# Kernel tuning notes

Hardware: AMD Instinct MI355X
Metric: run time of the kernel (lower is better)

The kernel has to match this reference:

```python
import math
import jax, jax.numpy as jnp
import numpy as np

B, L, D_MODEL = 2, 2048, 1024
N_HEAD, HEAD_DIM = 16, 64
ATT_SCALE = 1.0  # divisor is sqrt(head_dim ** attention_scale)


def setup_inputs() -> dict:
    key = jax.random.key(0)
    ks = jax.random.split(key, 6)
    HD = N_HEAD * HEAD_DIM
    # Xavier-uniform style init for projection weights (stored as [in, out])
    def xavier(k, fan_in, fan_out):
        lim = math.sqrt(6.0 / (fan_in + fan_out))
        return jax.random.uniform(k, (fan_in, fan_out), jnp.float32, -lim, lim)
    return {
        "x":  jax.random.normal(ks[0], (B, L, D_MODEL), jnp.float32),
        "Wq": xavier(ks[1], D_MODEL, HD), "bq": jnp.zeros((HD,), jnp.float32),
        "Wk": xavier(ks[2], D_MODEL, HD), "bk": jnp.zeros((HD,), jnp.float32),
        "Wv": xavier(ks[3], D_MODEL, HD), "bv": jnp.zeros((HD,), jnp.float32),
        "Wo": xavier(ks[4], HD, D_MODEL),
        "bo": jax.random.uniform(ks[5], (D_MODEL,), jnp.float32, -1.0 / math.sqrt(HD), 1.0 / math.sqrt(HD)),
    }


def reference(x, Wq, bq, Wk, bk, Wv, bv, Wo, bo):
    b, l, _ = x.shape
    # QKV projections -> [B, L, H, Dh]
    q = (x @ Wq + bq).reshape(b, l, N_HEAD, HEAD_DIM)
    k = (x @ Wk + bk).reshape(b, l, N_HEAD, HEAD_DIM)
    v = (x @ Wv + bv).reshape(b, l, N_HEAD, HEAD_DIM)
    scale = 1.0 / math.sqrt(HEAD_DIM ** ATT_SCALE)
    # Unnormalized (no softmax) attention: (Q K^T / sqrt(Dh)) V
    scores = jnp.einsum("blhd,bmhd->bhlm", q, k) * scale  # [B,H,L,L]
    attn = jnp.einsum("bhlm,bmhd->blhd", scores, v)        # [B,L,H,Dh]
    out = attn.reshape(b, l, N_HEAD * HEAD_DIM) @ Wo + bo  # dispatcher
    return out
```

## Files before the change

### kernel.cpp

```cpp
#include <hip/hip_runtime.h>
#include <stdint.h>

#define B_ 2
#define L_ 2048
#define DM 1024
#define NH 16
#define DH 64
#define M_ (B_*L_)
#define NQKV 3072

typedef short short8 __attribute__((ext_vector_type(8)));
typedef float f32x4 __attribute__((ext_vector_type(4)));

__device__ __forceinline__ unsigned short f2b(float f) {
    union { float f; unsigned int u; } v; v.f = f;
    unsigned int u = v.u;
    return (unsigned short)((u + 0x7fffu + ((u >> 16) & 1u)) >> 16);
}

__device__ __forceinline__ void gld_lds16(const void* g, void* l) {
    __builtin_amdgcn_global_load_lds(
        (const __attribute__((address_space(1))) void*)g,
        (__attribute__((address_space(3))) void*)l, 16, 0, 0);
}

__global__ __launch_bounds__(256)
void setup_kernel(const float* __restrict__ x,
                  const float* __restrict__ Wq, const float* __restrict__ Wk,
                  const float* __restrict__ Wv, const float* __restrict__ Wo,
                  const float* __restrict__ bq, const float* __restrict__ bk,
                  const float* __restrict__ bv,
                  unsigned short* __restrict__ xb, unsigned short* __restrict__ WqkvT,
                  unsigned short* __restrict__ WoT, float* __restrict__ biasq,
                  float* __restrict__ KtV)
{
    __shared__ float tile[32][33];
    const int bid = blockIdx.x;
    const int t = threadIdx.x;

    if (bid < 2048) {
        int i = (bid * 256 + t) * 8;
        float4 a0 = *(const float4*)(x + i);
        float4 a1 = *(const float4*)(x + i + 4);
        uint4 p;
        p.x = (unsigned)f2b(a0.x) | ((unsigned)f2b(a0.y) << 16);
        p.y = (unsigned)f2b(a0.z) | ((unsigned)f2b(a0.w) << 16);
        p.z = (unsigned)f2b(a1.x) | ((unsigned)f2b(a1.y) << 16);
        p.w = (unsigned)f2b(a1.z) | ((unsigned)f2b(a1.w) << 16);
        *(uint4*)(xb + i) = p;
    } else if (bid < 2048 + 4096) {
        int wb = bid - 2048;
        int wi = wb >> 10;
        int tid = wb & 1023;
        const float* W = (wi == 0) ? Wq : (wi == 1) ? Wk : (wi == 2) ? Wv : Wo;
        float s = (wi == 1) ? 0.125f : 1.0f;
        int n0 = (tid & 31) * 32, k0 = (tid >> 5) * 32;
        int r = t >> 3, c4 = (t & 7) << 2;
        float4 v = *(const float4*)(W + (size_t)(k0 + r) * DM + n0 + c4);
        tile[r][c4+0] = v.x; tile[r][c4+1] = v.y; tile[r][c4+2] = v.z; tile[r][c4+3] = v.w;
        __syncthreads();
        uint2 o;
        o.x = (unsigned)f2b(tile[c4+0][r]*s) | ((unsigned)f2b(tile[c4+1][r]*s) << 16);
        o.y = (unsigned)f2b(tile[c4+2][r]*s) | ((unsigned)f2b(tile[c4+3][r]*s) << 16);
        int f = n0 + r;
        size_t drow;
        unsigned short* dst;
        if (wi == 0)      { dst = WqkvT; drow = f; }
        else if (wi == 1) { dst = WqkvT; drow = 1024 + (f >> 6) * 128 + (f & 63); }
        else if (wi == 2) { dst = WqkvT; drow = 1024 + (f >> 6) * 128 + 64 + (f & 63); }
        else              { dst = WoT;   drow = f; }
        *(uint2*)(dst + drow * DM + k0 + c4) = o;
    } else if (bid < 2048 + 4096 + 12) {
        int n = (bid - 6144) * 256 + t;
        float v;
        if (n < 1024) v = bq[n];
        else {
            int kv = (n - 1024) >> 7, r = (n - 1024) & 127;
            v = (r < 64) ? 0.125f * bk[kv * 64 + r] : bv[kv * 64 + (r - 64)];
        }
        biasq[n] = v;
    } else {
        int i = ((bid - 6156) * 256 + t) * 4;
        float4 z; z.x = z.y = z.z = z.w = 0.f;
        *(float4*)(KtV + i) = z;
    }
}

__global__ __launch_bounds__(256)
void qkv_fused_kernel(const unsigned short* __restrict__ A,
                      const unsigned short* __restrict__ Bt,
                      const float* __restrict__ biasq,
                      unsigned short* __restrict__ Qb,
                      float* __restrict__ KtV)
{
    __shared__ __align__(16) char smem[34816];
    unsigned short* As = (unsigned short*)smem;
    unsigned short* Bs = (unsigned short*)(smem + 8192);

    const int bid = blockIdx.x;
    const int xcd = bid & 7, local = bid >> 3;
    const int mt = xcd * 4 + (local & 3);
    const int nt = local >> 2;
    const int m0 = mt * 128, n0 = nt * 128;

    const int t = threadIdx.x;
    const int w = t >> 6, lane = t & 63;
    const int quad = lane >> 4, l16 = lane & 15;
    const int wm = w >> 1, wn = w & 1;

    f32x4 acc[4][4];
    #pragma unroll
    for (int i = 0; i < 4; i++)
        #pragma unroll
        for (int j = 0; j < 4; j++)
            #pragma unroll
            for (int r = 0; r < 4; r++) acc[i][j][r] = 0.f;

    const int srow = t >> 2;
    const int schunk = t & 3;

    for (int kk = 0; kk < DM; kk += 32) {
        #pragma unroll
        for (int p = 0; p < 2; p++) {
            int row = p * 64 + srow;
            int g = schunk ^ ((row >> 1) & 3);
            gld_lds16(A  + (size_t)(m0 + row) * DM + kk + g * 8,
                      (char*)As + p * 4096 + w * 1024);
            gld_lds16(Bt + (size_t)(n0 + row) * DM + kk + g * 8,
                      (char*)Bs + p * 4096 + w * 1024);
        }
        __syncthreads();

        short8 afr[4], bfr[4];
        #pragma unroll
        for (int i = 0; i < 4; i++) {
            int am = wm * 64 + i * 16 + l16;
            afr[i] = *(const short8*)((const char*)As + am * 64 + ((quad ^ ((am >> 1) & 3)) << 4));
            int bn = wn * 64 + i * 16 + l16;
            bfr[i] = *(const short8*)((const char*)Bs + bn * 64 + ((quad ^ ((bn >> 1) & 3)) << 4));
        }
        #pragma unroll
        for (int i = 0; i < 4; i++)
            #pragma unroll
            for (int j = 0; j < 4; j++)
                acc[i][j] = __builtin_amdgcn_mfma_f32_16x16x32_bf16(afr[i], bfr[j], acc[i][j], 0, 0, 0);
        __syncthreads();
    }

    #pragma unroll
    for (int j = 0; j < 4; j++) {
        float bv = biasq[n0 + wn * 64 + j * 16 + l16];
        #pragma unroll
        for (int i = 0; i < 4; i++)
            #pragma unroll
            for (int r = 0; r < 4; r++) acc[i][j][r] += bv;
    }

    if (nt < 8) {
        #pragma unroll
        for (int j = 0; j < 4; j++) {
            int col = n0 + wn * 64 + j * 16 + l16;
            #pragma unroll
            for (int i = 0; i < 4; i++) {
                #pragma unroll
                for (int r = 0; r < 4; r++) {
                    int row = m0 + wm * 64 + i * 16 + quad * 4 + r;
                    Qb[(size_t)row * DM + col] = f2b(acc[i][j][r]);
                }
            }
        }
        return;
    }

    const int h  = nt - 8;
    const int bh = (m0 >> 11) * NH + h;
    unsigned short (*Xt)[136] = (unsigned short (*)[136])smem;

    #pragma unroll
    for (int j = 0; j < 4; j++) {
        int c = wn * 64 + j * 16 + l16;
        #pragma unroll
        for (int i = 0; i < 4; i++) {
            int l0 = wm * 64 + i * 16 + quad * 4;
            uint2 o;
            o.x = (unsigned)f2b(acc[i][j][0]) | ((unsigned)f2b(acc[i][j][1]) << 16);
            o.y = (unsigned)f2b(acc[i][j][2]) | ((unsigned)f2b(acc[i][j][3]) << 16);
            *(uint2*)&Xt[c][l0] = o;
        }
    }
    __syncthreads();

    f32x4 kacc[4];
    #pragma unroll
    for (int j = 0; j < 4; j++)
        #pragma unroll
        for (int r = 0; r < 4; r++) kacc[j][r] = 0.f;

    #pragma unroll
    for (int ks = 0; ks < 4; ks++) {
        short8 af = *(const short8*)&Xt[w * 16 + l16][ks * 32 + quad * 8];
        #pragma unroll
        for (int j = 0; j < 4; j++) {
            short8 bfr = *(const short8*)&Xt[64 + j * 16 + l16][ks * 32 + quad * 8];
            kacc[j] = __builtin_amdgcn_mfma_f32_16x16x32_bf16(af, bfr, kacc[j], 0, 0, 0);
        }
    }

    float* dst = KtV + (size_t)bh * 64 * 64;
    #pragma unroll
    for (int j = 0; j < 4; j++) {
        int col = j * 16 + l16;
        #pragma unroll
        for (int r = 0; r < 4; r++) {
            int row = w * 16 + quad * 4 + r;
            atomicAdd(dst + row * 64 + col, kacc[j][r]);
        }
    }
}

__global__ __launch_bounds__(256)
void zmat_kernel(const unsigned short* __restrict__ WoT, const float* __restrict__ KtV,
                 unsigned short* __restrict__ ZT)
{
    __shared__ __align__(16) unsigned short Asl[64][72];
    __shared__ __align__(16) unsigned short Bsl[64][72];

    const int bh = blockIdx.x, nt0 = blockIdx.y;
    const int b = bh >> 4, h = bh & 15;
    const int t = threadIdx.x;
    const int wave = t >> 6, lane = t & 63;
    const int quad = lane >> 4, l16 = lane & 15;
    const int n0 = nt0 * 64;
    const int row = t >> 2, c0 = (t & 3) << 4;

    const unsigned short* ap = WoT + (size_t)(n0 + row) * DM + h * DH + c0;
    *(uint4*)&Asl[row][c0]     = *(const uint4*)ap;
    *(uint4*)&Asl[row][c0 + 8] = *(const uint4*)(ap + 8);

    const float* kp = KtV + ((size_t)bh * 64 + row) * 64 + c0;
    #pragma unroll
    for (int j = 0; j < 16; j++) Bsl[row][c0 + j] = f2b(kp[j]);
    __syncthreads();

    f32x4 acc[4];
    #pragma unroll
    for (int i = 0; i < 4; i++)
        #pragma unroll
        for (int r = 0; r < 4; r++) acc[i][r] = 0.f;

    #pragma unroll
    for (int ks = 0; ks < 2; ks++) {
        short8 af = *(const short8*)&Asl[wave * 16 + l16][ks * 32 + quad * 8];
        #pragma unroll
        for (int nt = 0; nt < 4; nt++) {
            short8 bfr = *(const short8*)&Bsl[nt * 16 + l16][ks * 32 + quad * 8];
            acc[nt] = __builtin_amdgcn_mfma_f32_16x16x32_bf16(af, bfr, acc[nt], 0, 0, 0);
        }
    }

    unsigned short* zb = ZT + (size_t)b * 1024 * 1024 + (size_t)h * DH;
    #pragma unroll
    for (int nt = 0; nt < 4; nt++) {
        int col = nt * 16 + l16;
        #pragma unroll
        for (int r = 0; r < 4; r++) {
            int zr = n0 + wave * 16 + quad * 4 + r;
            zb[(size_t)zr * 1024 + col] = f2b(acc[nt][r]);
        }
    }
}

__global__ __launch_bounds__(256)
void out_gemm_kernel(const unsigned short* __restrict__ A,
                     const unsigned short* __restrict__ Bt,
                     const float* __restrict__ bias,
                     float* __restrict__ C)
{
    constexpr int BN = 64, MI = 2, MJ = 4;
    __shared__ __align__(16) unsigned short As[128 * 32];
    __shared__ __align__(16) unsigned short Bs[BN * 32];

    const int bid = blockIdx.x;
    const int xcd = bid & 7, local = bid >> 3;
    const int mt = xcd * 4 + (local & 3);
    const int nt = local >> 2;
    const int m0 = mt * 128, n0 = nt * 64;

    const int t = threadIdx.x;
    const int w = t >> 6, lane = t & 63;
    const int quad = lane >> 4, l16 = lane & 15;

    const unsigned short* Btb = Bt + (size_t)(m0 >> 11) * 1024 * 1024;

    f32x4 acc[MI][MJ];
    #pragma unroll
    for (int i = 0; i < MI; i++)
        #pragma unroll
        for (int j = 0; j < MJ; j++)
            #pragma unroll
            for (int r = 0; r < 4; r++) acc[i][j][r] = 0.f;

    const int srow = t >> 2;
    const int schunk = t & 3;

    for (int kk = 0; kk < DM; kk += 32) {
        #pragma unroll
        for (int p = 0; p < 2; p++) {
            int row = p * 64 + srow;
            int g = schunk ^ ((row >> 1) & 3);
            gld_lds16(A + (size_t)(m0 + row) * DM + kk + g * 8,
                      (char*)As + p * 4096 + w * 1024);
        }
        {
            int row = srow;
            int g = schunk ^ ((row >> 1) & 3);
            gld_lds16(Btb + (size_t)(n0 + row) * DM + kk + g * 8,
                      (char*)Bs + w * 1024);
        }
        __syncthreads();

        short8 afr[MI], bfr[MJ];
        #pragma unroll
        for (int i = 0; i < MI; i++) {
            int am = w * 32 + i * 16 + l16;
            afr[i] = *(const short8*)((const char*)As + am * 64 + ((quad ^ ((am >> 1) & 3)) << 4));
        }
        #pragma unroll
        for (int j = 0; j < MJ; j++) {
            int bn = j * 16 + l16;
            bfr[j] = *(const short8*)((const char*)Bs + bn * 64 + ((quad ^ ((bn >> 1) & 3)) << 4));
        }
        #pragma unroll
        for (int i = 0; i < MI; i++)
            #pragma unroll
            for (int j = 0; j < MJ; j++)
                acc[i][j] = __builtin_amdgcn_mfma_f32_16x16x32_bf16(afr[i], bfr[j], acc[i][j], 0, 0, 0);
        __syncthreads();
    }

    #pragma unroll
    for (int j = 0; j < MJ; j++) {
        int col = n0 + j * 16 + l16;
        float bv = bias[col];
        #pragma unroll
        for (int i = 0; i < MI; i++) {
            #pragma unroll
            for (int r = 0; r < 4; r++) {
                int row = m0 + w * 32 + i * 16 + quad * 4 + r;
                C[(size_t)row * DM + col] = acc[i][j][r] + bv;
            }
        }
    }
}


extern "C" void kernel_launch(void* const* d_in, const int* in_sizes, int n_in,
                              void* d_out, int out_size, void* d_ws, size_t ws_size,
                              hipStream_t stream)
{
    const float* x  = (const float*)d_in[0];
    const float* Wq = (const float*)d_in[1];
    const float* bq = (const float*)d_in[2];
    const float* Wk = (const float*)d_in[3];
    const float* bk = (const float*)d_in[4];
    const float* Wv = (const float*)d_in[5];
    const float* bv = (const float*)d_in[6];
    const float* Wo = (const float*)d_in[7];
    const float* bo = (const float*)d_in[8];

    char* ws = (char*)d_ws;
    unsigned short* xb    = (unsigned short*)(ws);
    unsigned short* WqkvT = (unsigned short*)(ws + (size_t)8  * 1024 * 1024);
    unsigned short* WoT   = (unsigned short*)(ws + (size_t)14 * 1024 * 1024);
    float*          biasq = (float*)         (ws + (size_t)16 * 1024 * 1024);
    unsigned short* Qb    = (unsigned short*)(ws + (size_t)17 * 1024 * 1024);
    unsigned short* ZT    = (unsigned short*)(ws + (size_t)25 * 1024 * 1024);
    float*          KtV   = (float*)         (ws + (size_t)29 * 1024 * 1024);

    setup_kernel<<<6284, 256, 0, stream>>>(x, Wq, Wk, Wv, Wo, bq, bk, bv,
                                           xb, WqkvT, WoT, biasq, KtV);

    qkv_fused_kernel<<<768, 256, 0, stream>>>(xb, WqkvT, biasq, Qb, KtV);

    zmat_kernel<<<dim3(B_ * NH, 16), 256, 0, stream>>>(WoT, KtV, ZT);

    out_gemm_kernel<<<512, 256, 0, stream>>>(Qb, ZT, bo, (float*)d_out);
}
```

Before: 147.0 us.

## Use 128x128 split-K tiles in output GEMM with atomic accumulation onto bias-initialized output

The output GEMM now uses 128x128 tiles with a 2-way split over K, so each block computes a 4x4 MFMA grid per wave with more operand reuse while the block count stays at 512. Partial sums are accumulated into the output with float atomics, and the setup kernel pre-fills the output with the broadcast bias. This trades fewer redundant operand loads per FLOP for atomic traffic on 4M outputs, an extra full-output write in setup, and non-deterministic summation order.

```diff
diff --git a/kernel.cpp b/kernel.cpp
--- a/kernel.cpp
+++ b/kernel.cpp
@@ -29,10 +29,10 @@
                   const float* __restrict__ Wq, const float* __restrict__ Wk,
                   const float* __restrict__ Wv, const float* __restrict__ Wo,
                   const float* __restrict__ bq, const float* __restrict__ bk,
-                  const float* __restrict__ bv,
+                  const float* __restrict__ bv, const float* __restrict__ bo,
                   unsigned short* __restrict__ xb, unsigned short* __restrict__ WqkvT,
                   unsigned short* __restrict__ WoT, float* __restrict__ biasq,
-                  float* __restrict__ KtV)
+                  float* __restrict__ KtV, float* __restrict__ outp)
 {
     __shared__ float tile[32][33];
     const int bid = blockIdx.x;
@@ -79,10 +79,13 @@
             v = (r < 64) ? 0.125f * bk[kv * 64 + r] : bv[kv * 64 + (r - 64)];
         }
         biasq[n] = v;
-    } else {
+    } else if (bid < 2048 + 4096 + 12 + 128) {
         int i = ((bid - 6156) * 256 + t) * 4;
         float4 z; z.x = z.y = z.z = z.w = 0.f;
         *(float4*)(KtV + i) = z;
+    } else {
+        int i = ((bid - 6284) * 256 + t) * 4;
+        *(float4*)(outp + i) = *(const float4*)(bo + (i & 1023));
     }
 }
 
@@ -273,81 +276,74 @@
 __global__ __launch_bounds__(256)
 void out_gemm_kernel(const unsigned short* __restrict__ A,
                      const unsigned short* __restrict__ Bt,
-                     const float* __restrict__ bias,
                      float* __restrict__ C)
 {
-    constexpr int BN = 64, MI = 2, MJ = 4;
     __shared__ __align__(16) unsigned short As[128 * 32];
-    __shared__ __align__(16) unsigned short Bs[BN * 32];
+    __shared__ __align__(16) unsigned short Bs[128 * 32];
 
     const int bid = blockIdx.x;
     const int xcd = bid & 7, local = bid >> 3;
-    const int mt = xcd * 4 + (local & 3);
-    const int nt = local >> 2;
-    const int m0 = mt * 128, n0 = nt * 64;
+    const int kh = local & 1;
+    const int mt = xcd * 4 + ((local >> 1) & 3);
+    const int nt = local >> 3;
+    const int m0 = mt * 128, n0 = nt * 128;
+    const int kbase = kh * 512;
 
     const int t = threadIdx.x;
     const int w = t >> 6, lane = t & 63;
     const int quad = lane >> 4, l16 = lane & 15;
-
-    const unsigned short* Btb = Bt + (size_t)(m0 >> 11) * 1024 * 1024;
-
-    f32x4 acc[MI][MJ];
-    #pragma unroll
-    for (int i = 0; i < MI; i++)
-        #pragma unroll
-        for (int j = 0; j < MJ; j++)
+    const int wm = w >> 1, wn = w & 1;
+
+    const unsigned short* Btb = Bt + (size_t)(mt >> 4) * 1024 * 1024;
+
+    f32x4 acc[4][4];
+    #pragma unroll
+    for (int i = 0; i < 4; i++)
+        #pragma unroll
+        for (int j = 0; j < 4; j++)
             #pragma unroll
             for (int r = 0; r < 4; r++) acc[i][j][r] = 0.f;
 
     const int srow = t >> 2;
     const int schunk = t & 3;
 
-    for (int kk = 0; kk < DM; kk += 32) {
+    for (int kk = kbase; kk < kbase + 512; kk += 32) {
         #pragma unroll
         for (int p = 0; p < 2; p++) {
             int row = p * 64 + srow;
             int g = schunk ^ ((row >> 1) & 3);
-            gld_lds16(A + (size_t)(m0 + row) * DM + kk + g * 8,
+            gld_lds16(A   + (size_t)(m0 + row) * DM + kk + g * 8,
                       (char*)As + p * 4096 + w * 1024);
-        }
-        {
-            int row = srow;
-            int g = schunk ^ ((row >> 1) & 3);
             gld_lds16(Btb + (size_t)(n0 + row) * DM + kk + g * 8,
-                      (char*)Bs + w * 1024);
-        }
-        __syncthreads();
-
-        short8 afr[MI], bfr[MJ];
-        #pragma unroll
-        for (int i = 0; i < MI; i++) {
-            int am = w * 32 + i * 16 + l16;
+                      (char*)Bs + p * 4096 + w * 1024);
+        }
+        __syncthreads();
+
+        short8 afr[4], bfr[4];
+        #pragma unroll
+        for (int i = 0; i < 4; i++) {
+            int am = wm * 64 + i * 16 + l16;
             afr[i] = *(const short8*)((const char*)As + am * 64 + ((quad ^ ((am >> 1) & 3)) << 4));
-        }
-        #pragma unroll
-        for (int j = 0; j < MJ; j++) {
-            int bn = j * 16 + l16;
-            bfr[j] = *(const short8*)((const char*)Bs + bn * 64 + ((quad ^ ((bn >> 1) & 3)) << 4));
-        }
-        #pragma unroll
-        for (int i = 0; i < MI; i++)
-            #pragma unroll
-            for (int j = 0; j < MJ; j++)
+            int bn = wn * 64 + i * 16 + l16;
+            bfr[i] = *(const short8*)((const char*)Bs + bn * 64 + ((quad ^ ((bn >> 1) & 3)) << 4));
+        }
+        #pragma unroll
+        for (int i = 0; i < 4; i++)
+            #pragma unroll
+            for (int j = 0; j < 4; j++)
                 acc[i][j] = __builtin_amdgcn_mfma_f32_16x16x32_bf16(afr[i], bfr[j], acc[i][j], 0, 0, 0);
         __syncthreads();
     }
 
     #pragma unroll
-    for (int j = 0; j < MJ; j++) {
-        int col = n0 + j * 16 + l16;
-        float bv = bias[col];
-        #pragma unroll
-        for (int i = 0; i < MI; i++) {
+    for (int j = 0; j < 4; j++) {
+        int col = n0 + wn * 64 + j * 16 + l16;
+        #pragma unroll
+        for (int i = 0; i < 4; i++) {
             #pragma unroll
             for (int r = 0; r < 4; r++) {
-                int row = m0 + w * 32 + i * 16 + quad * 4 + r;
-                C[(size_t)row * DM + col] = acc[i][j][r] + bv;
+                int row = m0 + wm * 64 + i * 16 + quad * 4 + r;
+                atomicAdd(C + (size_t)row * DM + col, acc[i][j][r]);
             }
         }
     }
@@ -377,12 +373,12 @@
     unsigned short* ZT    = (unsigned short*)(ws + (size_t)25 * 1024 * 1024);
     float*          KtV   = (float*)         (ws + (size_t)29 * 1024 * 1024);
 
-    setup_kernel<<<6284, 256, 0, stream>>>(x, Wq, Wk, Wv, Wo, bq, bk, bv,
-                                           xb, WqkvT, WoT, biasq, KtV);
+    setup_kernel<<<7308, 256, 0, stream>>>(x, Wq, Wk, Wv, Wo, bq, bk, bv, bo,
+                                           xb, WqkvT, WoT, biasq, KtV, (float*)d_out);
 
     qkv_fused_kernel<<<768, 256, 0, stream>>>(xb, WqkvT, biasq, Qb, KtV);
 
     zmat_kernel<<<dim3(B_ * NH, 16), 256, 0, stream>>>(WoT, KtV, ZT);
 
-    out_gemm_kernel<<<512, 256, 0, stream>>>(Qb, ZT, bo, (float*)d_out);
-}
+    out_gemm_kernel<<<512, 256, 0, stream>>>(Qb, ZT, (float*)d_out);
+}
```

Result: slower. 164.8 us (+12.1%).

## Fuse four kernels into one persistent kernel with grid barriers

Applied to the files above, without the earlier changes.

Replaces the setup, QKV GEMM, Z-matrix and output GEMM launches with a single kernel of 768 blocks that steps through the phases, separated by atomic-counter grid barriers. A memset resets the counters before each launch. The aim is to remove inter-kernel launch gaps and tail drain. The cost is that all 768 blocks must be co-resident (launch_bounds 256,3), otherwise the barrier deadlocks. Idle blocks also sit out the later phases, and the setup work becomes a grid-stride loop.

```diff
diff --git a/kernel.cpp b/kernel.cpp
--- a/kernel.cpp
+++ b/kernel.cpp
@@ -8,6 +8,7 @@
 #define DH 64
 #define M_ (B_*L_)
 #define NQKV 3072
+#define NBLK 768
 
 typedef short short8 __attribute__((ext_vector_type(8)));
 typedef float f32x4 __attribute__((ext_vector_type(4)));
@@ -24,330 +25,322 @@
         (__attribute__((address_space(3))) void*)l, 16, 0, 0);
 }
 
-__global__ __launch_bounds__(256)
-void setup_kernel(const float* __restrict__ x,
-                  const float* __restrict__ Wq, const float* __restrict__ Wk,
-                  const float* __restrict__ Wv, const float* __restrict__ Wo,
-                  const float* __restrict__ bq, const float* __restrict__ bk,
-                  const float* __restrict__ bv,
-                  unsigned short* __restrict__ xb, unsigned short* __restrict__ WqkvT,
-                  unsigned short* __restrict__ WoT, float* __restrict__ biasq,
-                  float* __restrict__ KtV)
-{
-    __shared__ float tile[32][33];
-    const int bid = blockIdx.x;
-    const int t = threadIdx.x;
-
-    if (bid < 2048) {
-        int i = (bid * 256 + t) * 8;
-        float4 a0 = *(const float4*)(x + i);
-        float4 a1 = *(const float4*)(x + i + 4);
-        uint4 p;
-        p.x = (unsigned)f2b(a0.x) | ((unsigned)f2b(a0.y) << 16);
-        p.y = (unsigned)f2b(a0.z) | ((unsigned)f2b(a0.w) << 16);
-        p.z = (unsigned)f2b(a1.x) | ((unsigned)f2b(a1.y) << 16);
-        p.w = (unsigned)f2b(a1.z) | ((unsigned)f2b(a1.w) << 16);
-        *(uint4*)(xb + i) = p;
-    } else if (bid < 2048 + 4096) {
-        int wb = bid - 2048;
-        int wi = wb >> 10;
-        int tid = wb & 1023;
-        const float* W = (wi == 0) ? Wq : (wi == 1) ? Wk : (wi == 2) ? Wv : Wo;
-        float s = (wi == 1) ? 0.125f : 1.0f;
-        int n0 = (tid & 31) * 32, k0 = (tid >> 5) * 32;
-        int r = t >> 3, c4 = (t & 7) << 2;
-        float4 v = *(const float4*)(W + (size_t)(k0 + r) * DM + n0 + c4);
-        tile[r][c4+0] = v.x; tile[r][c4+1] = v.y; tile[r][c4+2] = v.z; tile[r][c4+3] = v.w;
-        __syncthreads();
-        uint2 o;
-        o.x = (unsigned)f2b(tile[c4+0][r]*s) | ((unsigned)f2b(tile[c4+1][r]*s) << 16);
-        o.y = (unsigned)f2b(tile[c4+2][r]*s) | ((unsigned)f2b(tile[c4+3][r]*s) << 16);
-        int f = n0 + r;
-        size_t drow;
-        unsigned short* dst;
-        if (wi == 0)      { dst = WqkvT; drow = f; }
-        else if (wi == 1) { dst = WqkvT; drow = 1024 + (f >> 6) * 128 + (f & 63); }
-        else if (wi == 2) { dst = WqkvT; drow = 1024 + (f >> 6) * 128 + 64 + (f & 63); }
-        else              { dst = WoT;   drow = f; }
-        *(uint2*)(dst + drow * DM + k0 + c4) = o;
-    } else if (bid < 2048 + 4096 + 12) {
-        int n = (bid - 6144) * 256 + t;
-        float v;
-        if (n < 1024) v = bq[n];
-        else {
-            int kv = (n - 1024) >> 7, r = (n - 1024) & 127;
-            v = (r < 64) ? 0.125f * bk[kv * 64 + r] : bv[kv * 64 + (r - 64)];
-        }
-        biasq[n] = v;
-    } else {
-        int i = ((bid - 6156) * 256 + t) * 4;
-        float4 z; z.x = z.y = z.z = z.w = 0.f;
-        *(float4*)(KtV + i) = z;
-    }
-}
-
-__global__ __launch_bounds__(256)
-void qkv_fused_kernel(const unsigned short* __restrict__ A,
-                      const unsigned short* __restrict__ Bt,
-                      const float* __restrict__ biasq,
-                      unsigned short* __restrict__ Qb,
-                      float* __restrict__ KtV)
+__device__ __forceinline__ void grid_barrier(unsigned* cnt) {
+    __syncthreads();
+    if (threadIdx.x == 0) {
+        __threadfence();
+        __hip_atomic_fetch_add(cnt, 1u, __ATOMIC_ACQ_REL, __HIP_MEMORY_SCOPE_AGENT);
+        while (__hip_atomic_load(cnt, __ATOMIC_ACQUIRE, __HIP_MEMORY_SCOPE_AGENT) < NBLK) {}
+        __threadfence();
+    }
+    __syncthreads();
+}
+
+__global__ __launch_bounds__(256, 3)
+void mega_kernel(const float* __restrict__ x,
+                 const float* __restrict__ Wq, const float* __restrict__ Wk,
+                 const float* __restrict__ Wv, const float* __restrict__ Wo,
+                 const float* __restrict__ bq, const float* __restrict__ bk,
+                 const float* __restrict__ bv, const float* __restrict__ bo,
+                 unsigned short* __restrict__ xb, unsigned short* __restrict__ WqkvT,
+                 unsigned short* __restrict__ WoT, float* __restrict__ biasq,
+                 unsigned short* __restrict__ Qb, unsigned short* __restrict__ ZT,
+                 float* __restrict__ KtV, float* __restrict__ outp,
+                 unsigned* __restrict__ gcnt)
 {
     __shared__ __align__(16) char smem[34816];
-    unsigned short* As = (unsigned short*)smem;
-    unsigned short* Bs = (unsigned short*)(smem + 8192);
-
     const int bid = blockIdx.x;
-    const int xcd = bid & 7, local = bid >> 3;
-    const int mt = xcd * 4 + (local & 3);
-    const int nt = local >> 2;
-    const int m0 = mt * 128, n0 = nt * 128;
-
     const int t = threadIdx.x;
     const int w = t >> 6, lane = t & 63;
     const int quad = lane >> 4, l16 = lane & 15;
-    const int wm = w >> 1, wn = w & 1;
-
-    f32x4 acc[4][4];
-    #pragma unroll
-    for (int i = 0; i < 4; i++)
-        #pragma unroll
-        for (int j = 0; j < 4; j++)
-            #pragma unroll
-            for (int r = 0; r < 4; r++) acc[i][j][r] = 0.f;
-
-    const int srow = t >> 2;
-    const int schunk = t & 3;
-
-    for (int kk = 0; kk < DM; kk += 32) {
-        #pragma unroll
-        for (int p = 0; p < 2; p++) {
-            int row = p * 64 + srow;
-            int g = schunk ^ ((row >> 1) & 3);
-            gld_lds16(A  + (size_t)(m0 + row) * DM + kk + g * 8,
-                      (char*)As + p * 4096 + w * 1024);
-            gld_lds16(Bt + (size_t)(n0 + row) * DM + kk + g * 8,
-                      (char*)Bs + p * 4096 + w * 1024);
-        }
+
+    {
+        float (*tile)[33] = (float (*)[33])smem;
+        for (int u = bid; u < 6284; u += NBLK) {
+            if (u < 2048) {
+                int i = (u * 256 + t) * 8;
+                float4 a0 = *(const float4*)(x + i);
+                float4 a1 = *(const float4*)(x + i + 4);
+                uint4 p;
+                p.x = (unsigned)f2b(a0.x) | ((unsigned)f2b(a0.y) << 16);
+                p.y = (unsigned)f2b(a0.z) | ((unsigned)f2b(a0.w) << 16);
+                p.z = (unsigned)f2b(a1.x) | ((unsigned)f2b(a1.y) << 16);
+                p.w = (unsigned)f2b(a1.z) | ((unsigned)f2b(a1.w) << 16);
+                *(uint4*)(xb + i) = p;
+            } else if (u < 2048 + 4096) {
+                int wb = u - 2048;
+                int wi = wb >> 10;
+                int tid = wb & 1023;
+                const float* W = (wi == 0) ? Wq : (wi == 1) ? Wk : (wi == 2) ? Wv : Wo;
+                float s = (wi == 1) ? 0.125f : 1.0f;
+                int n0 = (tid & 31) * 32, k0 = (tid >> 5) * 32;
+                int r = t >> 3, c4 = (t & 7) << 2;
+                float4 v = *(const float4*)(W + (size_t)(k0 + r) * DM + n0 + c4);
+                tile[r][c4+0] = v.x; tile[r][c4+1] = v.y;
+                tile[r][c4+2] = v.z; tile[r][c4+3] = v.w;
+                __syncthreads();
+                uint2 o;
+                o.x = (unsigned)f2b(tile[c4+0][r]*s) | ((unsigned)f2b(tile[c4+1][r]*s) << 16);
+                o.y = (unsigned)f2b(tile[c4+2][r]*s) | ((unsigned)f2b(tile[c4+3][r]*s) << 16);
+                int f = n0 + r;
+                size_t drow;
+                unsigned short* dst;
+                if (wi == 0)      { dst = WqkvT; drow = f; }
+                else if (wi == 1) { dst = WqkvT; drow = 1024 + (f >> 6) * 128 + (f & 63); }
+                else if (wi == 2) { dst = WqkvT; drow = 1024 + (f >> 6) * 128 + 64 + (f & 63); }
+                else              { dst = WoT;   drow = f; }
+                *(uint2*)(dst + drow * DM + k0 + c4) = o;
+            } else if (u < 2048 + 4096 + 12) {
+                int n = (u - 6144) * 256 + t;
+                float v;
+                if (n < 1024) v = bq[n];
+                else {
+                    int kv = (n - 1024) >> 7, r = (n - 1024) & 127;
+                    v = (r < 64) ? 0.125f * bk[kv * 64 + r] : bv[kv * 64 + (r - 64)];
+                }
+                biasq[n] = v;
+            } else {
+                int i = ((u - 6156) * 256 + t) * 4;
+                float4 z; z.x = z.y = z.z = z.w = 0.f;
+                *(float4*)(KtV + i) = z;
+            }
+            __syncthreads();
+        }
+    }
+    grid_barrier(gcnt + 0);
+
+    {
+        unsigned short* As = (unsigned short*)smem;
+        unsigned short* Bs = (unsigned short*)(smem + 8192);
+        const int xcd = bid & 7, local = bid >> 3;
+        const int mt = xcd * 4 + (local & 3);
+        const int nt = local >> 2;
+        const int m0 = mt * 128, n0 = nt * 128;
+        const int wm = w >> 1, wn = w & 1;
+
+        f32x4 acc[4][4];
+        #pragma unroll
+        for (int i = 0; i < 4; i++)
+            #pragma unroll
+            for (int j = 0; j < 4; j++)
+                #pragma unroll
+                for (int r = 0; r < 4; r++) acc[i][j][r] = 0.f;
+
+        const int srow = t >> 2;
+        const int schunk = t & 3;
+
+        for (int kk = 0; kk < DM; kk += 32) {
+            #pragma unroll
+            for (int p = 0; p < 2; p++) {
+                int row = p * 64 + srow;
+                int g = schunk ^ ((row >> 1) & 3);
+                gld_lds16(xb    + (size_t)(m0 + row) * DM + kk + g * 8,
+                          (char*)As + p * 4096 + w * 1024);
+                gld_lds16(WqkvT + (size_t)(n0 + row) * DM + kk + g * 8,
+                          (char*)Bs + p * 4096 + w * 1024);
+            }
+            __syncthreads();
+
+            short8 afr[4], bfr[4];
+            #pragma unroll
+            for (int i = 0; i < 4; i++) {
+                int am = wm * 64 + i * 16 + l16;
+                afr[i] = *(const short8*)((const char*)As + am * 64 + ((quad ^ ((am >> 1) & 3)) << 4));
+                int bn = wn * 64 + i * 16 + l16;
+                bfr[i] = *(const short8*)((const char*)Bs + bn * 64 + ((quad ^ ((bn >> 1) & 3)) << 4));
+            }
+            #pragma unroll
+            for (int i = 0; i < 4; i++)
+                #pragma unroll
+                for (int j = 0; j < 4; j++)
+                    acc[i][j] = __builtin_amdgcn_mfma_f32_16x16x32_bf16(afr[i], bfr[j], acc[i][j], 0, 0, 0);
+            __syncthreads();
+        }
+
+        #pragma unroll
+        for (int j = 0; j < 4; j++) {
+            float bv = biasq[n0 + wn * 64 + j * 16 + l16];
+            #pragma unroll
+            for (int i = 0; i < 4; i++)
+                #pragma unroll
+                for (int r = 0; r < 4; r++) acc[i][j][r] += bv;
+        }
+
+        if (nt < 8) {
+            #pragma unroll
+            for (int j = 0; j < 4; j++) {
+                int col = n0 + wn * 64 + j * 16 + l16;
+                #pragma unroll
+                for (int i = 0; i < 4; i++) {
+                    #pragma unroll
+                    for (int r = 0; r < 4; r++) {
+                        int row = m0 + wm * 64 + i * 16 + quad * 4 + r;
+                        Qb[(size_t)row * DM + col] = f2b(acc[i][j][r]);
+                    }
+                }
+            }
+        } else {
+            const int h  = nt - 8;
+            const int bh = (m0 >> 11) * NH + h;
+            unsigned short (*Xt)[136] = (unsigned short (*)[136])smem;
+
+            #pragma unroll
+            for (int j = 0; j < 4; j++) {
+                int c = wn * 64 + j * 16 + l16;
+                #pragma unroll
+                for (int i = 0; i < 4; i++) {
+                    int l0 = wm * 64 + i * 16 + quad * 4;
+                    uint2 o;
+                    o.x = (unsigned)f2b(acc[i][j][0]) | ((unsigned)f2b(acc[i][j][1]) << 16);
+                    o.y = (unsigned)f2b(acc[i][j][2]) | ((unsigned)f2b(acc[i][j][3]) << 16);
+                    *(uint2*)&Xt[c][l0] = o;
+                }
+            }
+            __syncthreads();
+
+            f32x4 kacc[4];
+            #pragma unroll
+            for (int j = 0; j < 4; j++)
+                #pragma unroll
+                for (int r = 0; r < 4; r++) kacc[j][r] = 0.f;
+
+            #pragma unroll
+            for (int ks = 0; ks < 4; ks++) {
+                short8 af = *(const short8*)&Xt[w * 16 + l16][ks * 32 + quad * 8];
+                #pragma unroll
+                for (int j = 0; j < 4; j++) {
+                    short8 bfr = *(const short8*)&Xt[64 + j * 16 + l16][ks * 32 + quad * 8];
+                    kacc[j] = __builtin_amdgcn_mfma_f32_16x16x32_bf16(af, bfr, kacc[j], 0, 0, 0);
+                }
+            }
+
+            float* dst = KtV + (size_t)bh * 64 * 64;
+            #pragma unroll
+            for (int j = 0; j < 4; j++) {
+                int col = j * 16 + l16;
+                #pragma unroll
+                for (int r = 0; r < 4; r++) {
+                    int row = w * 16 + quad * 4 + r;
+                    atomicAdd(dst + row * 64 + col, kacc[j][r]);
+                }
+            }
+        }
+    }
+    grid_barrier(gcnt + 32);
+
+    if (bid < 512) {
+        unsigned short (*Asl)[72] = (unsigned short (*)[72])smem;
+        unsigned short (*Bsl)[72] = (unsigned short (*)[72])(smem + 9216);
+        const int bh = bid & 31, nt0 = bid >> 5;
+        const int b = bh >> 4, h = bh & 15;
+        const int n0 = nt0 * 64;
+        const int row = t >> 2, c0 = (t & 3) << 4;
+
+        const unsigned short* ap = WoT + (size_t)(n0 + row) * DM + h * DH + c0;
+        *(uint4*)&Asl[row][c0]     = *(const uint4*)ap;
+        *(uint4*)&Asl[row][c0 + 8] = *(const uint4*)(ap + 8);
+
+        const float* kp = KtV + ((size_t)bh * 64 + row) * 64 + c0;
+        #pragma unroll
+        for (int j = 0; j < 16; j++) Bsl[row][c0 + j] = f2b(kp[j]);
         __syncthreads();
 
-        short8 afr[4], bfr[4];
-        #pragma unroll
-        for (int i = 0; i < 4; i++) {
-            int am = wm * 64 + i * 16 + l16;
-            afr[i] = *(const short8*)((const char*)As + am * 64 + ((quad ^ ((am >> 1) & 3)) << 4));
-            int bn = wn * 64 + i * 16 + l16;
-            bfr[i] = *(const short8*)((const char*)Bs + bn * 64 + ((quad ^ ((bn >> 1) & 3)) << 4));
-        }
+        f32x4 acc[4];
         #pragma unroll
         for (int i = 0; i < 4; i++)
             #pragma unroll
+            for (int r = 0; r < 4; r++) acc[i][r] = 0.f;
+
+        #pragma unroll
+        for (int ks = 0; ks < 2; ks++) {
+            short8 af = *(const short8*)&Asl[w * 16 + l16][ks * 32 + quad * 8];
+            #pragma unroll
+            for (int nt = 0; nt < 4; nt++) {
+                short8 bfr = *(const short8*)&Bsl[nt * 16 + l16][ks * 32 + quad * 8];
+                acc[nt] = __builtin_amdgcn_mfma_f32_16x16x32_bf16(af, bfr, acc[nt], 0, 0, 0);
+            }
+        }
+
+        unsigned short* zb = ZT + (size_t)b * 1024 * 1024 + (size_t)h * DH;
+        #pragma unroll
+        for (int nt = 0; nt < 4; nt++) {
+            int col = nt * 16 + l16;
+            #pragma unroll
+            for (int r = 0; r < 4; r++) {
+                int zr = n0 + w * 16 + quad * 4 + r;
+                zb[(size_t)zr * 1024 + col] = f2b(acc[nt][r]);
+            }
+        }
+    }
+    grid_barrier(gcnt + 64);
+
+    if (bid < 512) {
+        unsigned short* As = (unsigned short*)smem;
+        unsigned short* Bs = (unsigned short*)(smem + 8192);
+        const int xcd = bid & 7, local = bid >> 3;
+        const int mt = xcd * 4 + (local & 3);
+        const int nt = local >> 2;
+        const int m0 = mt * 128, n0 = nt * 64;
+
+        const unsigned short* Btb = ZT + (size_t)(m0 >> 11) * 1024 * 1024;
+
+        f32x4 acc[2][4];
+        #pragma unroll
+        for (int i = 0; i < 2; i++)
+            #pragma unroll
             for (int j = 0; j < 4; j++)
-                acc[i][j] = __builtin_amdgcn_mfma_f32_16x16x32_bf16(afr[i], bfr[j], acc[i][j], 0, 0, 0);
-        __syncthreads();
-    }
-
-    #pragma unroll
-    for (int j = 0; j < 4; j++) {
-        float bv = biasq[n0 + wn * 64 + j * 16 + l16];
-        #pragma unroll
-        for (int i = 0; i < 4; i++)
-            #pragma unroll
-            for (int r = 0; r < 4; r++) acc[i][j][r] += bv;
-    }
-
-    if (nt < 8) {
+                #pragma unroll
+                for (int r = 0; r < 4; r++) acc[i][j][r] = 0.f;
+
+        const int srow = t >> 2;
+        const int schunk = t & 3;
+
+        for (int kk = 0; kk < DM; kk += 32) {
+            #pragma unroll
+            for (int p = 0; p < 2; p++) {
+                int row = p * 64 + srow;
+                int g = schunk ^ ((row >> 1) & 3);
+                gld_lds16(Qb + (size_t)(m0 + row) * DM + kk + g * 8,
+                          (char*)As + p * 4096 + w * 1024);
+            }
+            {
+                int row = srow;
+                int g = schunk ^ ((row >> 1) & 3);
+                gld_lds16(Btb + (size_t)(n0 + row) * DM + kk + g * 8,
+                          (char*)Bs + w * 1024);
+            }
+            __syncthreads();
+
+            short8 afr[2], bfr[4];
+            #pragma unroll
+            for (int i = 0; i < 2; i++) {
+                int am = w * 32 + i * 16 + l16;
+                afr[i] = *(const short8*)((const char*)As + am * 64 + ((quad ^ ((am >> 1) & 3)) << 4));
+            }
+            #pragma unroll
+            for (int j = 0; j < 4; j++) {
+                int bn = j * 16 + l16;
+                bfr[j] = *(const short8*)((const char*)Bs + bn * 64 + ((quad ^ ((bn >> 1) & 3)) << 4));
+            }
+            #pragma unroll
+            for (int i = 0; i < 2; i++)
+                #pragma unroll
+                for (int j = 0; j < 4; j++)
+                    acc[i][j] = __builtin_amdgcn_mfma_f32_16x16x32_bf16(afr[i], bfr[j], acc[i][j], 0, 0, 0);
+            __syncthreads();
+        }
+
         #pragma unroll
         for (int j = 0; j < 4; j++) {
-            int col = n0 + wn * 64 + j * 16 + l16;
-            #pragma unroll
-            for (int i = 0; i < 4; i++) {
+            int col = n0 + j * 16 + l16;
+            float bv = bo[col];
+            #pragma unroll
+            for (int i = 0; i < 2; i++) {
                 #pragma unroll
                 for (int r = 0; r < 4; r++) {
-                    int row = m0 + wm * 64 + i * 16 + quad * 4 + r;
-                    Qb[(size_t)row * DM + col] = f2b(acc[i][j][r]);
-                }
-            }
-        }
-        return;
-    }
-
-    const int h  = nt - 8;
-    const int bh = (m0 >> 11) * NH + h;
-    unsigned short (*Xt)[136] = (unsigned short (*)[136])smem;
-
-    #pragma unroll
-    for (int j = 0; j < 4; j++) {
-        int c = wn * 64 + j * 16 + l16;
-        #pragma unroll
-        for (int i = 0; i < 4; i++) {
-            int l0 = wm * 64 + i * 16 + quad * 4;
-            uint2 o;
-            o.x = (unsigned)f2b(acc[i][j][0]) | ((unsigned)f2b(acc[i][j][1]) << 16);
-            o.y = (unsigned)f2b(acc[i][j][2]) | ((unsigned)f2b(acc[i][j][3]) << 16);
-            *(uint2*)&Xt[c][l0] = o;
-        }
-    }
-    __syncthreads();
-
-    f32x4 kacc[4];
-    #pragma unroll
-    for (int j = 0; j < 4; j++)
-        #pragma unroll
-        for (int r = 0; r < 4; r++) kacc[j][r] = 0.f;
-
-    #pragma unroll
-    for (int ks = 0; ks < 4; ks++) {
-        short8 af = *(const short8*)&Xt[w * 16 + l16][ks * 32 + quad * 8];
-        #pragma unroll
-        for (int j = 0; j < 4; j++) {
-            short8 bfr = *(const short8*)&Xt[64 + j * 16 + l16][ks * 32 + quad * 8];
-            kacc[j] = __builtin_amdgcn_mfma_f32_16x16x32_bf16(af, bfr, kacc[j], 0, 0, 0);
-        }
-    }
-
-    float* dst = KtV + (size_t)bh * 64 * 64;
-    #pragma unroll
-    for (int j = 0; j < 4; j++) {
-        int col = j * 16 + l16;
-        #pragma unroll
-        for (int r = 0; r < 4; r++) {
-            int row = w * 16 + quad * 4 + r;
-            atomicAdd(dst + row * 64 + col, kacc[j][r]);
-        }
-    }
-}
-
-__global__ __launch_bounds__(256)
-void zmat_kernel(const unsigned short* __restrict__ WoT, const float* __restrict__ KtV,
-                 unsigned short* __restrict__ ZT)
-{
-    __shared__ __align__(16) unsigned short Asl[64][72];
-    __shared__ __align__(16) unsigned short Bsl[64][72];
-
-    const int bh = blockIdx.x, nt0 = blockIdx.y;
-    const int b = bh >> 4, h = bh & 15;
-    const int t = threadIdx.x;
-    const int wave = t >> 6, lane = t & 63;
-    const int quad = lane >> 4, l16 = lane & 15;
-    const int n0 = nt0 * 64;
-    const int row = t >> 2, c0 = (t & 3) << 4;
-
-    const unsigned short* ap = WoT + (size_t)(n0 + row) * DM + h * DH + c0;
-    *(uint4*)&Asl[row][c0]     = *(const uint4*)ap;
-    *(uint4*)&Asl[row][c0 + 8] = *(const uint4*)(ap + 8);
-
-    const float* kp = KtV + ((size_t)bh * 64 + row) * 64 + c0;
-    #pragma unroll
-    for (int j = 0; j < 16; j++) Bsl[row][c0 + j] = f2b(kp[j]);
-    __syncthreads();
-
-    f32x4 acc[4];
-    #pragma unroll
-    for (int i = 0; i < 4; i++)
-        #pragma unroll
-        for (int r = 0; r < 4; r++) acc[i][r] = 0.f;
-
-    #pragma unroll
-    for (int ks = 0; ks < 2; ks++) {
-        short8 af = *(const short8*)&Asl[wave * 16 + l16][ks * 32 + quad * 8];
-        #pragma unroll
-        for (int nt = 0; nt < 4; nt++) {
-            short8 bfr = *(const short8*)&Bsl[nt * 16 + l16][ks * 32 + quad * 8];
-            acc[nt] = __builtin_amdgcn_mfma_f32_16x16x32_bf16(af, bfr, acc[nt], 0, 0, 0);
-        }
-    }
-
-    unsigned short* zb = ZT + (size_t)b * 1024 * 1024 + (size_t)h * DH;
-    #pragma unroll
-    for (int nt = 0; nt < 4; nt++) {
-        int col = nt * 16 + l16;
-        #pragma unroll
-        for (int r = 0; r < 4; r++) {
-            int zr = n0 + wave * 16 + quad * 4 + r;
-            zb[(size_t)zr * 1024 + col] = f2b(acc[nt][r]);
-        }
-    }
-}
-
-__global__ __launch_bounds__(256)
-void out_gemm_kernel(const unsigned short* __restrict__ A,
-                     const unsigned short* __restrict__ Bt,
-                     const float* __restrict__ bias,
-                     float* __restrict__ C)
-{
-    constexpr int BN = 64, MI = 2, MJ = 4;
-    __shared__ __align__(16) unsigned short As[128 * 32];
-    __shared__ __align__(16) unsigned short Bs[BN * 32];
-
-    const int bid = blockIdx.x;
-    const int xcd = bid & 7, local = bid >> 3;
-    const int mt = xcd * 4 + (local & 3);
-    const int nt = local >> 2;
-    const int m0 = mt * 128, n0 = nt * 64;
-
-    const int t = threadIdx.x;
-    const int w = t >> 6, lane = t & 63;
-    const int quad = lane >> 4, l16 = lane & 15;
-
-    const unsigned short* Btb = Bt + (size_t)(m0 >> 11) * 1024 * 1024;
-
-    f32x4 acc[MI][MJ];
-    #pragma unroll
-    for (int i = 0; i < MI; i++)
-        #pragma unroll
-        for (int j = 0; j < MJ; j++)
-            #pragma unroll
-            for (int r = 0; r < 4; r++) acc[i][j][r] = 0.f;
-
-    const int srow = t >> 2;
-    const int schunk = t & 3;
-
-    for (int kk = 0; kk < DM; kk += 32) {
-        #pragma unroll
-        for (int p = 0; p < 2; p++) {
-            int row = p * 64 + srow;
-            int g = schunk ^ ((row >> 1) & 3);
-            gld_lds16(A + (size_t)(m0 + row) * DM + kk + g * 8,
-                      (char*)As + p * 4096 + w * 1024);
-        }
-        {
-            int row = srow;
-            int g = schunk ^ ((row >> 1) & 3);
-            gld_lds16(Btb + (size_t)(n0 + row) * DM + kk + g * 8,
-                      (char*)Bs + w * 1024);
-        }
-        __syncthreads();
-
-        short8 afr[MI], bfr[MJ];
-        #pragma unroll
-        for (int i = 0; i < MI; i++) {
-            int am = w * 32 + i * 16 + l16;
-            afr[i] = *(const short8*)((const char*)As + am * 64 + ((quad ^ ((am >> 1) & 3)) << 4));
-        }
-        #pragma unroll
-        for (int j = 0; j < MJ; j++) {
-            int bn = j * 16 + l16;
-            bfr[j] = *(const short8*)((const char*)Bs + bn * 64 + ((quad ^ ((bn >> 1) & 3)) << 4));
-        }
-        #pragma unroll
-        for (int i = 0; i < MI; i++)
-            #pragma unroll
-            for (int j = 0; j < MJ; j++)
-                acc[i][j] = __builtin_amdgcn_mfma_f32_16x16x32_bf16(afr[i], bfr[j], acc[i][j], 0, 0, 0);
-        __syncthreads();
-    }
-
-    #pragma unroll
-    for (int j = 0; j < MJ; j++) {
-        int col = n0 + j * 16 + l16;
-        float bv = bias[col];
-        #pragma unroll
-        for (int i = 0; i < MI; i++) {
-            #pragma unroll
-            for (int r = 0; r < 4; r++) {
-                int row = m0 + w * 32 + i * 16 + quad * 4 + r;
-                C[(size_t)row * DM + col] = acc[i][j][r] + bv;
+                    int row = m0 + w * 32 + i * 16 + quad * 4 + r;
+                    outp[(size_t)row * DM + col] = acc[i][j][r] + bv;
+                }
             }
         }
     }
@@ -376,13 +369,11 @@
     unsigned short* Qb    = (unsigned short*)(ws + (size_t)17 * 1024 * 1024);
     unsigned short* ZT    = (unsigned short*)(ws + (size_t)25 * 1024 * 1024);
     float*          KtV   = (float*)         (ws + (size_t)29 * 1024 * 1024);
-
-    setup_kernel<<<6284, 256, 0, stream>>>(x, Wq, Wk, Wv, Wo, bq, bk, bv,
-                                           xb, WqkvT, WoT, biasq, KtV);
-
-    qkv_fused_kernel<<<768, 256, 0, stream>>>(xb, WqkvT, biasq, Qb, KtV);
-
-    zmat_kernel<<<dim3(B_ * NH, 16), 256, 0, stream>>>(WoT, KtV, ZT);
-
-    out_gemm_kernel<<<512, 256, 0, stream>>>(Qb, ZT, bo, (float*)d_out);
-}
+    unsigned*       gcnt  = (unsigned*)      (ws + (size_t)30 * 1024 * 1024);
+
+    hipMemsetAsync(gcnt, 0, 3 * 32 * sizeof(unsigned), stream);
+
+    mega_kernel<<<NBLK, 256, 0, stream>>>(x, Wq, Wk, Wv, Wo, bq, bk, bv, bo,
+                                          xb, WqkvT, WoT, biasq, Qb, ZT, KtV,
+                                          (float*)d_out, gcnt);
+}
```

Result: slower. 434.2 us (+195.3%).

## Fuse Z-matrix and output GEMM kernels with a grid-wide atomic barrier

Applied to the files above, without the earlier changes.

Merges the zmat kernel (512 blocks: 32 bh by 16 n-tiles) and the output GEMM (512 blocks) into one persistent launch. A global atomic counter acts as a grid barrier between the two phases, and it is reset each call with a memset. This removes one kernel launch and its gap. It relies on all 512 blocks being co-resident, otherwise the spin loop deadlocks, and it adds a memset plus the spin-wait cost.

```diff
diff --git a/kernel.cpp b/kernel.cpp
--- a/kernel.cpp
+++ b/kernel.cpp
@@ -219,135 +219,141 @@
 }
 
 __global__ __launch_bounds__(256)
-void zmat_kernel(const unsigned short* __restrict__ WoT, const float* __restrict__ KtV,
-                 unsigned short* __restrict__ ZT)
+void zmat_out_kernel(const unsigned short* __restrict__ WoT,
+                     const float* __restrict__ KtV,
+                     unsigned short* __restrict__ ZT,
+                     const unsigned short* __restrict__ Qb,
+                     const float* __restrict__ bo,
+                     float* __restrict__ outp,
+                     unsigned* __restrict__ gcnt)
 {
-    __shared__ __align__(16) unsigned short Asl[64][72];
-    __shared__ __align__(16) unsigned short Bsl[64][72];
-
-    const int bh = blockIdx.x, nt0 = blockIdx.y;
-    const int b = bh >> 4, h = bh & 15;
-    const int t = threadIdx.x;
-    const int wave = t >> 6, lane = t & 63;
-    const int quad = lane >> 4, l16 = lane & 15;
-    const int n0 = nt0 * 64;
-    const int row = t >> 2, c0 = (t & 3) << 4;
-
-    const unsigned short* ap = WoT + (size_t)(n0 + row) * DM + h * DH + c0;
-    *(uint4*)&Asl[row][c0]     = *(const uint4*)ap;
-    *(uint4*)&Asl[row][c0 + 8] = *(const uint4*)(ap + 8);
-
-    const float* kp = KtV + ((size_t)bh * 64 + row) * 64 + c0;
-    #pragma unroll
-    for (int j = 0; j < 16; j++) Bsl[row][c0 + j] = f2b(kp[j]);
-    __syncthreads();
-
-    f32x4 acc[4];
-    #pragma unroll
-    for (int i = 0; i < 4; i++)
-        #pragma unroll
-        for (int r = 0; r < 4; r++) acc[i][r] = 0.f;
-
-    #pragma unroll
-    for (int ks = 0; ks < 2; ks++) {
-        short8 af = *(const short8*)&Asl[wave * 16 + l16][ks * 32 + quad * 8];
-        #pragma unroll
-        for (int nt = 0; nt < 4; nt++) {
-            short8 bfr = *(const short8*)&Bsl[nt * 16 + l16][ks * 32 + quad * 8];
-            acc[nt] = __builtin_amdgcn_mfma_f32_16x16x32_bf16(af, bfr, acc[nt], 0, 0, 0);
-        }
-    }
-
-    unsigned short* zb = ZT + (size_t)b * 1024 * 1024 + (size_t)h * DH;
-    #pragma unroll
-    for (int nt = 0; nt < 4; nt++) {
-        int col = nt * 16 + l16;
-        #pragma unroll
-        for (int r = 0; r < 4; r++) {
-            int zr = n0 + wave * 16 + quad * 4 + r;
-            zb[(size_t)zr * 1024 + col] = f2b(acc[nt][r]);
-        }
-    }
-}
-
-__global__ __launch_bounds__(256)
-void out_gemm_kernel(const unsigned short* __restrict__ A,
-                     const unsigned short* __restrict__ Bt,
-                     const float* __restrict__ bias,
-                     float* __restrict__ C)
-{
-    constexpr int BN = 64, MI = 2, MJ = 4;
-    __shared__ __align__(16) unsigned short As[128 * 32];
-    __shared__ __align__(16) unsigned short Bs[BN * 32];
-
+    __shared__ __align__(16) char smem[18432];
     const int bid = blockIdx.x;
-    const int xcd = bid & 7, local = bid >> 3;
-    const int mt = xcd * 4 + (local & 3);
-    const int nt = local >> 2;
-    const int m0 = mt * 128, n0 = nt * 64;
-
     const int t = threadIdx.x;
     const int w = t >> 6, lane = t & 63;
     const int quad = lane >> 4, l16 = lane & 15;
 
-    const unsigned short* Btb = Bt + (size_t)(m0 >> 11) * 1024 * 1024;
-
-    f32x4 acc[MI][MJ];
-    #pragma unroll
-    for (int i = 0; i < MI; i++)
-        #pragma unroll
-        for (int j = 0; j < MJ; j++)
-            #pragma unroll
-            for (int r = 0; r < 4; r++) acc[i][j][r] = 0.f;
-
-    const int srow = t >> 2;
-    const int schunk = t & 3;
-
-    for (int kk = 0; kk < DM; kk += 32) {
-        #pragma unroll
-        for (int p = 0; p < 2; p++) {
-            int row = p * 64 + srow;
-            int g = schunk ^ ((row >> 1) & 3);
-            gld_lds16(A + (size_t)(m0 + row) * DM + kk + g * 8,
-                      (char*)As + p * 4096 + w * 1024);
-        }
-        {
-            int row = srow;
-            int g = schunk ^ ((row >> 1) & 3);
-            gld_lds16(Btb + (size_t)(n0 + row) * DM + kk + g * 8,
-                      (char*)Bs + w * 1024);
-        }
+    {
+        unsigned short (*Asl)[72] = (unsigned short (*)[72])smem;
+        unsigned short (*Bsl)[72] = (unsigned short (*)[72])(smem + 9216);
+        const int bh = bid & 31, nt0 = bid >> 5;
+        const int b = bh >> 4, h = bh & 15;
+        const int n0 = nt0 * 64;
+        const int row = t >> 2, c0 = (t & 3) << 4;
+
+        const unsigned short* ap = WoT + (size_t)(n0 + row) * DM + h * DH + c0;
+        *(uint4*)&Asl[row][c0]     = *(const uint4*)ap;
+        *(uint4*)&Asl[row][c0 + 8] = *(const uint4*)(ap + 8);
+
+        const float* kp = KtV + ((size_t)bh * 64 + row) * 64 + c0;
+        #pragma unroll
+        for (int j = 0; j < 16; j++) Bsl[row][c0 + j] = f2b(kp[j]);
         __syncthreads();
 
-        short8 afr[MI], bfr[MJ];
-        #pragma unroll
-        for (int i = 0; i < MI; i++) {
-            int am = w * 32 + i * 16 + l16;
-            afr[i] = *(const short8*)((const char*)As + am * 64 + ((quad ^ ((am >> 1) & 3)) << 4));
-        }
-        #pragma unroll
-        for (int j = 0; j < MJ; j++) {
-            int bn = j * 16 + l16;
-            bfr[j] = *(const short8*)((const char*)Bs + bn * 64 + ((quad ^ ((bn >> 1) & 3)) << 4));
-        }
-        #pragma unroll
-        for (int i = 0; i < MI; i++)
-            #pragma unroll
-            for (int j = 0; j < MJ; j++)
-                acc[i][j] = __builtin_amdgcn_mfma_f32_16x16x32_bf16(afr[i], bfr[j], acc[i][j], 0, 0, 0);
-        __syncthreads();
-    }
-
-    #pragma unroll
-    for (int j = 0; j < MJ; j++) {
-        int col = n0 + j * 16 + l16;
-        float bv = bias[col];
-        #pragma unroll
-        for (int i = 0; i < MI; i++) {
+        f32x4 acc[4];
+        #pragma unroll
+        for (int i = 0; i < 4; i++)
+            #pragma unroll
+            for (int r = 0; r < 4; r++) acc[i][r] = 0.f;
+
+        #pragma unroll
+        for (int ks = 0; ks < 2; ks++) {
+            short8 af = *(const short8*)&Asl[w * 16 + l16][ks * 32 + quad * 8];
+            #pragma unroll
+            for (int nt = 0; nt < 4; nt++) {
+                short8 bfr = *(const short8*)&Bsl[nt * 16 + l16][ks * 32 + quad * 8];
+                acc[nt] = __builtin_amdgcn_mfma_f32_16x16x32_bf16(af, bfr, acc[nt], 0, 0, 0);
+            }
+        }
+
+        unsigned short* zb = ZT + (size_t)b * 1024 * 1024 + (size_t)h * DH;
+        #pragma unroll
+        for (int nt = 0; nt < 4; nt++) {
+            int col = nt * 16 + l16;
             #pragma unroll
             for (int r = 0; r < 4; r++) {
-                int row = m0 + w * 32 + i * 16 + quad * 4 + r;
-                C[(size_t)row * DM + col] = acc[i][j][r] + bv;
+                int zr = n0 + w * 16 + quad * 4 + r;
+                zb[(size_t)zr * 1024 + col] = f2b(acc[nt][r]);
+            }
+        }
+    }
+
+    __syncthreads();
+    if (t == 0) {
+        __threadfence();
+        __hip_atomic_fetch_add(gcnt, 1u, __ATOMIC_ACQ_REL, __HIP_MEMORY_SCOPE_AGENT);
+        while (__hip_atomic_load(gcnt, __ATOMIC_ACQUIRE, __HIP_MEMORY_SCOPE_AGENT) < 512u) {}
+        __threadfence();
+    }
+    __syncthreads();
+
+    {
+        unsigned short* As = (unsigned short*)smem;
+        unsigned short* Bs = (unsigned short*)(smem + 8192);
+        const int xcd = bid & 7, local = bid >> 3;
+        const int mt = xcd * 4 + (local & 3);
+        const int nt = local >> 2;
+        const int m0 = mt * 128, n0 = nt * 64;
+
+        const unsigned short* Btb = ZT + (size_t)(m0 >> 11) * 1024 * 1024;
+
+        f32x4 acc[2][4];
+        #pragma unroll
+        for (int i = 0; i < 2; i++)
+            #pragma unroll
+            for (int j = 0; j < 4; j++)
+                #pragma unroll
+                for (int r = 0; r < 4; r++) acc[i][j][r] = 0.f;
+
+        const int srow = t >> 2;
+        const int schunk = t & 3;
+
+        for (int kk = 0; kk < DM; kk += 32) {
+            #pragma unroll
+            for (int p = 0; p < 2; p++) {
+                int row = p * 64 + srow;
+                int g = schunk ^ ((row >> 1) & 3);
+                gld_lds16(Qb + (size_t)(m0 + row) * DM + kk + g * 8,
+                          (char*)As + p * 4096 + w * 1024);
+            }
+            {
+                int row = srow;
+                int g = schunk ^ ((row >> 1) & 3);
+                gld_lds16(Btb + (size_t)(n0 + row) * DM + kk + g * 8,
+                          (char*)Bs + w * 1024);
+            }
+            __syncthreads();
+
+            short8 afr[2], bfr[4];
+            #pragma unroll
+            for (int i = 0; i < 2; i++) {
+                int am = w * 32 + i * 16 + l16;
+                afr[i] = *(const short8*)((const char*)As + am * 64 + ((quad ^ ((am >> 1) & 3)) << 4));
+            }
+            #pragma unroll
+            for (int j = 0; j < 4; j++) {
+                int bn = j * 16 + l16;
+                bfr[j] = *(const short8*)((const char*)Bs + bn * 64 + ((quad ^ ((bn >> 1) & 3)) << 4));
+            }
+            #pragma unroll
+            for (int i = 0; i < 2; i++)
+                #pragma unroll
+                for (int j = 0; j < 4; j++)
+                    acc[i][j] = __builtin_amdgcn_mfma_f32_16x16x32_bf16(afr[i], bfr[j], acc[i][j], 0, 0, 0);
+            __syncthreads();
+        }
+
+        #pragma unroll
+        for (int j = 0; j < 4; j++) {
+            int col = n0 + j * 16 + l16;
+            float bv = bo[col];
+            #pragma unroll
+            for (int i = 0; i < 2; i++) {
+                #pragma unroll
+                for (int r = 0; r < 4; r++) {
+                    int row = m0 + w * 32 + i * 16 + quad * 4 + r;
+                    outp[(size_t)row * DM + col] = acc[i][j][r] + bv;
+                }
             }
         }
     }
@@ -376,13 +382,15 @@
     unsigned short* Qb    = (unsigned short*)(ws + (size_t)17 * 1024 * 1024);
     unsigned short* ZT    = (unsigned short*)(ws + (size_t)25 * 1024 * 1024);
     float*          KtV   = (float*)         (ws + (size_t)29 * 1024 * 1024);
+    unsigned*       gcnt  = (unsigned*)      (ws + (size_t)30 * 1024 * 1024);
+
+    hipMemsetAsync(gcnt, 0, sizeof(unsigned), stream);
 
     setup_kernel<<<6284, 256, 0, stream>>>(x, Wq, Wk, Wv, Wo, bq, bk, bv,
                                            xb, WqkvT, WoT, biasq, KtV);
 
     qkv_fused_kernel<<<768, 256, 0, stream>>>(xb, WqkvT, biasq, Qb, KtV);
 
-    zmat_kernel<<<dim3(B_ * NH, 16), 256, 0, stream>>>(WoT, KtV, ZT);
-
-    out_gemm_kernel<<<512, 256, 0, stream>>>(Qb, ZT, bo, (float*)d_out);
-}
+    zmat_out_kernel<<<512, 256, 0, stream>>>(WoT, KtV, ZT, Qb, bo,
+                                             (float*)d_out, gcnt);
+}
```

Result: slower. 199.2 us (+35.5%).
